# Performance work log

Measured on AMD Instinct MI355X. Metric: run time of the kernel, lower is better.

The kernel has to match this reference:

```python
import jax, jax.numpy as jnp
import numpy as np

VOCAB = 50257   # vocab_size
BASE = 64       # base_dim
DD = 64         # domain_dim (hidden width of each tiny domain MLP)
ND = 16         # number of grown domains (<= max_domains=30)
B, S = 16, 8192
CORR_SCALE = 0.1  # correction scale from forward()


def setup_inputs() -> dict:
    key = jax.random.key(0)
    k1, k2, k3, k4, k5 = jax.random.split(key, 5)
    x = jax.random.randint(k1, (B, S), 0, VOCAB)
    # token -> domain assignment; values >= ND mean "no domain" (~half assigned)
    token_domain = jax.random.randint(k2, (VOCAB,), 0, 2 * ND)
    base_embed = jax.random.normal(k3, (VOCAB, BASE), dtype=jnp.float32) * 0.02
    W1 = jax.random.normal(k4, (ND, BASE, DD), dtype=jnp.float32) * 0.01
    W2 = jax.random.normal(k5, (ND, DD, BASE), dtype=jnp.float32) * 0.01
    return {"x": x, "token_domain": token_domain,
            "base_embed": base_embed, "W1": W1, "W2": W2}


def reference(x, token_domain, base_embed, W1, W2):
    # h: [B, S, BASE] base embedding lookup
    h = base_embed[x]
    d = token_domain[x]  # [B, S] domain id per token; >= ND -> unassigned
    out = h
    # Loop over the small fixed set of domains (MoE-style combine).
    # Each domain: Linear(no bias) -> exact GELU -> Linear(no bias), scaled by 0.1,
    # added only where the token belongs to that domain.
    for i in range(ND):
        hid = jax.nn.gelu(jnp.einsum('bsc,cd->bsd', h, W1[i]), approximate=False)
        corr = jnp.einsum('bsd,dc->bsc', hid, W2[i])
        out = out + jnp.where((d == i)[..., None], CORR_SCALE * corr, 0.0)
    return out
```

## Files before the change

kernel.cpp:

```cpp
#include <hip/hip_runtime.h>
#include <hip/hip_bf16.h>

#define VOCABSZ 50257
#define BASEDIM 64
#define ND 16
#define NTOK (16 * 8192)
#define CAP 4096
#define NBLK2 16
#define CNT_STRIDE 16

typedef __attribute__((ext_vector_type(8))) short short8;
typedef __attribute__((ext_vector_type(4))) float f32x4;

__device__ __forceinline__ short f2bf(float f) {
    union { float f; unsigned u; } v; v.f = f;
    unsigned r = (v.u + 0x7FFFu + ((v.u >> 16) & 1u)) >> 16;
    return (short)r;
}

__device__ __forceinline__ float bf2f(unsigned short b) {
    union { unsigned u; float f; } v; v.u = ((unsigned)b) << 16;
    return v.f;
}

__global__ __launch_bounds__(256) void k_vbucket(
    const int* __restrict__ tdom, const float* __restrict__ emb,
    unsigned short* __restrict__ table16, int* __restrict__ g_cnt,
    int* __restrict__ bucket)
{
    __shared__ int sm_d[256];
    __shared__ int sm_cnt[ND];
    __shared__ int sm_base[ND];

    const int lt = threadIdx.x;
    const int v0 = blockIdx.x * 256;
    const int v  = v0 + lt;

    if (lt < ND) sm_cnt[lt] = 0;
    __syncthreads();

    int d = 0x7fffffff;
    if (v < VOCABSZ) d = tdom[v];
    sm_d[lt] = d;
    int pos = -1;
    if (d < ND) pos = atomicAdd(&sm_cnt[d], 1);
    __syncthreads();

    if (lt < ND) sm_base[lt] = atomicAdd(&g_cnt[lt * CNT_STRIDE], sm_cnt[lt]);
    __syncthreads();

    if (d < ND) {
        const int gp = sm_base[d] + pos;
        if (gp < CAP) bucket[d * CAP + gp] = v;
    }

    const int g = lt >> 4, l16 = lt & 15;
    const float4* ev = (const float4*)emb;
    #pragma unroll
    for (int it = 0; it < 16; ++it) {
        const int li = it * 16 + g;
        const int vv = v0 + li;
        if (vv < VOCABSZ && sm_d[li] >= ND) {
            const float4 p = ev[(size_t)vv * 16 + l16];
            short4 s;
            s.x = f2bf(p.x); s.y = f2bf(p.y); s.z = f2bf(p.z); s.w = f2bf(p.w);
            *(short4*)&table16[(size_t)vv * 64 + l16 * 4] = s;
        }
    }
}

__global__ __launch_bounds__(256) void k_vcorrect(
    const float* __restrict__ emb, const float* __restrict__ W1,
    const float* __restrict__ W2, const int* __restrict__ g_cnt,
    const int* __restrict__ bucket, unsigned short* __restrict__ table16)
{
    const int blk   = blockIdx.x;
    const int d     = blk / NBLK2;
    const int chunk = blk % NBLK2;
    int cnt = g_cnt[d * CNT_STRIDE];
    if (cnt > CAP) cnt = CAP;

    const int wave = threadIdx.x >> 6;
    const int lane = threadIdx.x & 63;
    const int kr   = (lane >> 4) * 8;
    const int nco  = lane & 15;

    __shared__ float sw[2][4096];
    __shared__ __align__(16) short sm_hid[4][16 * 72];

    {
        const float4* w1v = (const float4*)(W1 + (size_t)d * 4096);
        const float4* w2v = (const float4*)(W2 + (size_t)d * 4096);
        float4* s1 = (float4*)sw[0];
        float4* s2 = (float4*)sw[1];
        for (int i = threadIdx.x; i < 1024; i += 256) {
            s1[i] = w1v[i];
            s2[i] = w2v[i];
        }
    }
    __syncthreads();

    short8 fw1[8], fw2[8];
    #pragma unroll
    for (int kt = 0; kt < 2; ++kt) {
        #pragma unroll
        for (int nt = 0; nt < 4; ++nt) {
            short8 a, b;
            #pragma unroll
            for (int i = 0; i < 8; ++i) {
                const int k = kt * 32 + kr + i;
                const int n = nt * 16 + nco;
                a[i] = f2bf(sw[0][k * 64 + n]);
                b[i] = f2bf(sw[1][k * 64 + n]);
            }
            fw1[kt * 4 + nt] = a;
            fw2[kt * 4 + nt] = b;
        }
    }

    short* hidb = &sm_hid[wave][0];
    const int* buck = bucket + (size_t)d * CAP;

    for (int base = chunk * 64; base < cnt; base += NBLK2 * 64) {
        const int s0 = base + wave * 16;
        int rem = cnt - s0;
        if (rem <= 0) continue;
        if (rem > 16) rem = 16;

        const int m_idx = s0 + (nco < rem ? nco : rem - 1);
        const int vm = buck[m_idx];
        const float* hrow = emb + (size_t)vm * 64;
        short8 ha[2];
        #pragma unroll
        for (int kt = 0; kt < 2; ++kt) {
            const float4* hv = (const float4*)(hrow + kt * 32 + kr);
            const float4 p = hv[0], q = hv[1];
            short8 t;
            t[0] = f2bf(p.x); t[1] = f2bf(p.y); t[2] = f2bf(p.z); t[3] = f2bf(p.w);
            t[4] = f2bf(q.x); t[5] = f2bf(q.y); t[6] = f2bf(q.z); t[7] = f2bf(q.w);
            ha[kt] = t;
        }

        f32x4 acc[4];
        #pragma unroll
        for (int nt = 0; nt < 4; ++nt) {
            acc[nt] = (f32x4){0.f, 0.f, 0.f, 0.f};
            acc[nt] = __builtin_amdgcn_mfma_f32_16x16x32_bf16(ha[0], fw1[nt],     acc[nt], 0, 0, 0);
            acc[nt] = __builtin_amdgcn_mfma_f32_16x16x32_bf16(ha[1], fw1[4 + nt], acc[nt], 0, 0, 0);
        }

        #pragma unroll
        for (int nt = 0; nt < 4; ++nt) {
            #pragma unroll
            for (int i = 0; i < 4; ++i) {
                const float v  = acc[nt][i];
                const float gv = 0.5f * v * (1.0f + erff(v * 0.70710678118f));
                const int  mm  = (lane >> 4) * 4 + i;
                const int  c   = nt * 16 + nco;
                hidb[mm * 72 + c] = f2bf(gv);
            }
        }
        asm volatile("s_waitcnt lgkmcnt(0)" ::: "memory");
        __builtin_amdgcn_sched_barrier(0);

        short8 pa[2];
        #pragma unroll
        for (int kt = 0; kt < 2; ++kt)
            pa[kt] = *(const short8*)&hidb[(lane & 15) * 72 + kt * 32 + kr];

        f32x4 acc2[4];
        #pragma unroll
        for (int nt = 0; nt < 4; ++nt) {
            acc2[nt] = (f32x4){0.f, 0.f, 0.f, 0.f};
            acc2[nt] = __builtin_amdgcn_mfma_f32_16x16x32_bf16(pa[0], fw2[nt],     acc2[nt], 0, 0, 0);
            acc2[nt] = __builtin_amdgcn_mfma_f32_16x16x32_bf16(pa[1], fw2[4 + nt], acc2[nt], 0, 0, 0);
        }

        #pragma unroll
        for (int i = 0; i < 4; ++i) {
            const int mm = (lane >> 4) * 4 + i;
            if (mm < rem) {
                const int vv = buck[s0 + mm];
                const float* hr = emb + (size_t)vv * 64;
                unsigned short* trow = table16 + (size_t)vv * 64;
                #pragma unroll
                for (int nt = 0; nt < 4; ++nt) {
                    const int c = nt * 16 + nco;
                    trow[c] = (unsigned short)f2bf(hr[c] + 0.1f * acc2[nt][i]);
                }
            }
        }
    }
}

__global__ __launch_bounds__(256) void k_gather(
    const int* __restrict__ x, const unsigned short* __restrict__ table16,
    float* __restrict__ out)
{
    const int stride = gridDim.x * 256;
    for (int u = blockIdx.x * 256 + threadIdx.x; u < NTOK * 8; u += stride) {
        const int row = u >> 3, l8 = u & 7;
        const int xr  = x[row];
        const short8 v = *(const short8*)&table16[(size_t)xr * 64 + l8 * 8];
        float4 a, b;
        a.x = bf2f((unsigned short)v[0]); a.y = bf2f((unsigned short)v[1]);
        a.z = bf2f((unsigned short)v[2]); a.w = bf2f((unsigned short)v[3]);
        b.x = bf2f((unsigned short)v[4]); b.y = bf2f((unsigned short)v[5]);
        b.z = bf2f((unsigned short)v[6]); b.w = bf2f((unsigned short)v[7]);
        float4* orow = (float4*)(out + (size_t)row * 64 + l8 * 8);
        orow[0] = a;
        orow[1] = b;
    }
}

extern "C" void kernel_launch(void* const* d_in, const int* in_sizes, int n_in,
                              void* d_out, int out_size, void* d_ws, size_t ws_size,
                              hipStream_t stream) {
    const int*   x    = (const int*)d_in[0];
    const int*   tdom = (const int*)d_in[1];
    const float* emb  = (const float*)d_in[2];
    const float* W1   = (const float*)d_in[3];
    const float* W2   = (const float*)d_in[4];
    float* out = (float*)d_out;

    int*            g_cnt   = (int*)d_ws;
    int*            bucket  = (int*)((char*)d_ws + 4096);
    unsigned short* table16 = (unsigned short*)((char*)d_ws + (1u << 20));

    hipMemsetAsync(d_ws, 0, ND * CNT_STRIDE * sizeof(int), stream);
    hipLaunchKernelGGL(k_vbucket, dim3((VOCABSZ + 255) / 256), dim3(256), 0,
                       stream, tdom, emb, table16, g_cnt, bucket);
    hipLaunchKernelGGL(k_vcorrect, dim3(ND * NBLK2), dim3(256), 0, stream,
                       emb, W1, W2, g_cnt, bucket, table16);
    hipLaunchKernelGGL(k_gather, dim3(2048), dim3(256), 0, stream,
                       x, table16, out);
}
```

Before: 108.7 us.

## Drop bucket kernel and memset; per-block shared-memory token lists and direct fp32 gather for unassigned

Removes the global memset and bucketing kernel. Each correction block now scans a strided vocab class for its own domain and builds a local token list in shared memory via atomics. The gather reads fp32 embeddings directly for unassigned tokens and only uses the bf16 table for domain tokens. This saves one launch, the memset and the bf16 conversion pass, at the cost of redundant tdom scans across 512 blocks and an extra tdom lookup per gathered token. LCAP=128 silently drops tokens if a domain/class bucket overflows (expected ~49 per bucket).

```diff
diff --git a/kernel.cpp b/kernel.cpp
--- a/kernel.cpp
+++ b/kernel.cpp
@@ -5,9 +5,8 @@
 #define BASEDIM 64
 #define ND 16
 #define NTOK (16 * 8192)
-#define CAP 4096
-#define NBLK2 16
-#define CNT_STRIDE 16
+#define NCLS 32
+#define LCAP 128
 
 typedef __attribute__((ext_vector_type(8))) short short8;
 typedef __attribute__((ext_vector_type(4))) float f32x4;
@@ -23,82 +22,52 @@
     return v.f;
 }
 
-__global__ __launch_bounds__(256) void k_vbucket(
+__global__ __launch_bounds__(256) void k_vcorrect(
     const int* __restrict__ tdom, const float* __restrict__ emb,
-    unsigned short* __restrict__ table16, int* __restrict__ g_cnt,
-    int* __restrict__ bucket)
+    const float* __restrict__ W1, const float* __restrict__ W2,
+    unsigned short* __restrict__ table16)
 {
-    __shared__ int sm_d[256];
-    __shared__ int sm_cnt[ND];
-    __shared__ int sm_base[ND];
-
-    const int lt = threadIdx.x;
-    const int v0 = blockIdx.x * 256;
-    const int v  = v0 + lt;
-
-    if (lt < ND) sm_cnt[lt] = 0;
-    __syncthreads();
-
-    int d = 0x7fffffff;
-    if (v < VOCABSZ) d = tdom[v];
-    sm_d[lt] = d;
-    int pos = -1;
-    if (d < ND) pos = atomicAdd(&sm_cnt[d], 1);
-    __syncthreads();
-
-    if (lt < ND) sm_base[lt] = atomicAdd(&g_cnt[lt * CNT_STRIDE], sm_cnt[lt]);
-    __syncthreads();
-
-    if (d < ND) {
-        const int gp = sm_base[d] + pos;
-        if (gp < CAP) bucket[d * CAP + gp] = v;
-    }
-
-    const int g = lt >> 4, l16 = lt & 15;
-    const float4* ev = (const float4*)emb;
-    #pragma unroll
-    for (int it = 0; it < 16; ++it) {
-        const int li = it * 16 + g;
-        const int vv = v0 + li;
-        if (vv < VOCABSZ && sm_d[li] >= ND) {
-            const float4 p = ev[(size_t)vv * 16 + l16];
-            short4 s;
-            s.x = f2bf(p.x); s.y = f2bf(p.y); s.z = f2bf(p.z); s.w = f2bf(p.w);
-            *(short4*)&table16[(size_t)vv * 64 + l16 * 4] = s;
-        }
-    }
-}
-
-__global__ __launch_bounds__(256) void k_vcorrect(
-    const float* __restrict__ emb, const float* __restrict__ W1,
-    const float* __restrict__ W2, const int* __restrict__ g_cnt,
-    const int* __restrict__ bucket, unsigned short* __restrict__ table16)
-{
-    const int blk   = blockIdx.x;
-    const int d     = blk / NBLK2;
-    const int chunk = blk % NBLK2;
-    int cnt = g_cnt[d * CNT_STRIDE];
-    if (cnt > CAP) cnt = CAP;
-
-    const int wave = threadIdx.x >> 6;
-    const int lane = threadIdx.x & 63;
+    const int blk = blockIdx.x;
+    const int d   = blk >> 5;
+    const int c   = blk & (NCLS - 1);
+
+    const int lt   = threadIdx.x;
+    const int wave = lt >> 6;
+    const int lane = lt & 63;
     const int kr   = (lane >> 4) * 8;
     const int nco  = lane & 15;
 
     __shared__ float sw[2][4096];
     __shared__ __align__(16) short sm_hid[4][16 * 72];
+    __shared__ int list[LCAP];
+    __shared__ int lcnt;
+
+    if (lt == 0) lcnt = 0;
 
     {
         const float4* w1v = (const float4*)(W1 + (size_t)d * 4096);
         const float4* w2v = (const float4*)(W2 + (size_t)d * 4096);
         float4* s1 = (float4*)sw[0];
         float4* s2 = (float4*)sw[1];
-        for (int i = threadIdx.x; i < 1024; i += 256) {
-            s1[i] = w1v[i];
-            s2[i] = w2v[i];
+        #pragma unroll
+        for (int i = 0; i < 4; ++i) {
+            s1[lt + 256 * i] = w1v[lt + 256 * i];
+            s2[lt + 256 * i] = w2v[lt + 256 * i];
         }
     }
     __syncthreads();
+
+    for (int i = lt; i * NCLS + c < VOCABSZ; i += 256) {
+        const int v = i * NCLS + c;
+        if (tdom[v] == d) {
+            const int p = atomicAdd(&lcnt, 1);
+            if (p < LCAP) list[p] = v;
+        }
+    }
+    __syncthreads();
+
+    int cnt = lcnt;
+    if (cnt > LCAP) cnt = LCAP;
 
     short8 fw1[8], fw2[8];
     #pragma unroll
@@ -119,16 +88,15 @@
     }
 
     short* hidb = &sm_hid[wave][0];
-    const int* buck = bucket + (size_t)d * CAP;
-
-    for (int base = chunk * 64; base < cnt; base += NBLK2 * 64) {
+
+    for (int base = 0; base < cnt; base += 64) {
         const int s0 = base + wave * 16;
         int rem = cnt - s0;
         if (rem <= 0) continue;
         if (rem > 16) rem = 16;
 
         const int m_idx = s0 + (nco < rem ? nco : rem - 1);
-        const int vm = buck[m_idx];
+        const int vm = list[m_idx];
         const float* hrow = emb + (size_t)vm * 64;
         short8 ha[2];
         #pragma unroll
@@ -156,8 +124,8 @@
                 const float v  = acc[nt][i];
                 const float gv = 0.5f * v * (1.0f + erff(v * 0.70710678118f));
                 const int  mm  = (lane >> 4) * 4 + i;
-                const int  c   = nt * 16 + nco;
-                hidb[mm * 72 + c] = f2bf(gv);
+                const int  cc  = nt * 16 + nco;
+                hidb[mm * 72 + cc] = f2bf(gv);
             }
         }
         asm volatile("s_waitcnt lgkmcnt(0)" ::: "memory");
@@ -180,13 +148,13 @@
         for (int i = 0; i < 4; ++i) {
             const int mm = (lane >> 4) * 4 + i;
             if (mm < rem) {
-                const int vv = buck[s0 + mm];
+                const int vv = list[s0 + mm];
                 const float* hr = emb + (size_t)vv * 64;
                 unsigned short* trow = table16 + (size_t)vv * 64;
                 #pragma unroll
                 for (int nt = 0; nt < 4; ++nt) {
-                    const int c = nt * 16 + nco;
-                    trow[c] = (unsigned short)f2bf(hr[c] + 0.1f * acc2[nt][i]);
+                    const int cc = nt * 16 + nco;
+                    trow[cc] = (unsigned short)f2bf(hr[cc] + 0.1f * acc2[nt][i]);
                 }
             }
         }
@@ -194,19 +162,26 @@
 }
 
 __global__ __launch_bounds__(256) void k_gather(
-    const int* __restrict__ x, const unsigned short* __restrict__ table16,
+    const int* __restrict__ x, const int* __restrict__ tdom,
+    const float* __restrict__ emb, const unsigned short* __restrict__ table16,
     float* __restrict__ out)
 {
     const int stride = gridDim.x * 256;
     for (int u = blockIdx.x * 256 + threadIdx.x; u < NTOK * 8; u += stride) {
         const int row = u >> 3, l8 = u & 7;
         const int xr  = x[row];
-        const short8 v = *(const short8*)&table16[(size_t)xr * 64 + l8 * 8];
         float4 a, b;
-        a.x = bf2f((unsigned short)v[0]); a.y = bf2f((unsigned short)v[1]);
-        a.z = bf2f((unsigned short)v[2]); a.w = bf2f((unsigned short)v[3]);
-        b.x = bf2f((unsigned short)v[4]); b.y = bf2f((unsigned short)v[5]);
-        b.z = bf2f((unsigned short)v[6]); b.w = bf2f((unsigned short)v[7]);
+        if (tdom[xr] < ND) {
+            const short8 v = *(const short8*)&table16[(size_t)xr * 64 + l8 * 8];
+            a.x = bf2f((unsigned short)v[0]); a.y = bf2f((unsigned short)v[1]);
+            a.z = bf2f((unsigned short)v[2]); a.w = bf2f((unsigned short)v[3]);
+            b.x = bf2f((unsigned short)v[4]); b.y = bf2f((unsigned short)v[5]);
+            b.z = bf2f((unsigned short)v[6]); b.w = bf2f((unsigned short)v[7]);
+        } else {
+            const float4* ev = (const float4*)(emb + (size_t)xr * 64 + l8 * 8);
+            a = ev[0];
+            b = ev[1];
+        }
         float4* orow = (float4*)(out + (size_t)row * 64 + l8 * 8);
         orow[0] = a;
         orow[1] = b;
@@ -223,15 +198,10 @@
     const float* W2   = (const float*)d_in[4];
     float* out = (float*)d_out;
 
-    int*            g_cnt   = (int*)d_ws;
-    int*            bucket  = (int*)((char*)d_ws + 4096);
-    unsigned short* table16 = (unsigned short*)((char*)d_ws + (1u << 20));
-
-    hipMemsetAsync(d_ws, 0, ND * CNT_STRIDE * sizeof(int), stream);
-    hipLaunchKernelGGL(k_vbucket, dim3((VOCABSZ + 255) / 256), dim3(256), 0,
-                       stream, tdom, emb, table16, g_cnt, bucket);
-    hipLaunchKernelGGL(k_vcorrect, dim3(ND * NBLK2), dim3(256), 0, stream,
-                       emb, W1, W2, g_cnt, bucket, table16);
+    unsigned short* table16 = (unsigned short*)d_ws;
+
+    hipLaunchKernelGGL(k_vcorrect, dim3(ND * NCLS), dim3(256), 0, stream,
+                       tdom, emb, W1, W2, table16);
     hipLaunchKernelGGL(k_gather, dim3(2048), dim3(256), 0, stream,
-                       x, table16, out);
-}
+                       x, tdom, emb, table16, out);
+}
```

After: 98.15 us. 1.11x faster.
